# Kernel tuning notes

Hardware: AMD Instinct MI355X
Metric: run time of the kernel (lower is better)

Reference implementation:

```python
import jax, jax.numpy as jnp
import numpy as np


def setup_inputs() -> dict:
    key = jax.random.key(0)
    ks = jax.random.split(key, 8)
    B, C, H, W = 8, 256, 64, 64
    s = 1.0 / np.sqrt(C)
    return {
        "x": jax.random.normal(ks[0], (B, C, H, W), dtype=jnp.float32),
        "wq": jax.random.normal(ks[1], (C, C), dtype=jnp.float32) * s,
        "bq": jax.random.normal(ks[2], (C,), dtype=jnp.float32) * 0.01,
        "wk": jax.random.normal(ks[3], (C, C), dtype=jnp.float32) * s,
        "bk": jax.random.normal(ks[4], (C,), dtype=jnp.float32) * 0.01,
        "wv": jax.random.normal(ks[5], (C, C), dtype=jnp.float32) * s,
        "bv": jax.random.normal(ks[6], (C,), dtype=jnp.float32) * 0.01,
        "gamma": jax.random.normal(ks[7], (1,), dtype=jnp.float32) * 0.1,
    }


def reference(x, wq, bq, wk, bk, wv, bv, gamma):
    B, C, H, W = x.shape
    N = H * W
    xf = x.reshape(B, C, N)  # flatten spatial -> tokens
    # 1x1 convs == per-pixel linear maps over channels
    q = jnp.einsum('oc,bcn->bon', wq, xf) + bq[None, :, None]  # [B,C,N]
    k = jnp.einsum('oc,bcn->bon', wk, xf) + bk[None, :, None]  # [B,C,N]
    v = jnp.einsum('oc,bcn->bon', wv, xf) + bv[None, :, None]  # [B,C,N]
    # energy[b,n,m] = <q[:, n], k[:, m]>  (query tokens x key tokens)
    energy = jnp.einsum('bcn,bcm->bnm', q, k)  # [B,N,N]
    attention = jax.nn.softmax(energy, axis=-1)
    # out = V @ attention^T : out[b,c,n] = sum_m v[b,c,m] * attention[b,n,m]
    out = jnp.einsum('bcm,bnm->bcn', v, attention).reshape(B, C, H, W)
    return gamma[0] * out + x
```

## Files before the change

kernel.cpp:

```cpp
#include <hip/hip_runtime.h>
#include <hip/hip_bf16.h>
#include <cstdint>


typedef short short8 __attribute__((ext_vector_type(8)));
typedef short short4v __attribute__((ext_vector_type(4)));
typedef float f32x4 __attribute__((ext_vector_type(4)));

#define MFMA16(a, b, c) __builtin_amdgcn_mfma_f32_16x16x32_bf16((a), (b), (c), 0, 0, 0)

__device__ __forceinline__ unsigned short f2bf(float f) {
    union { float f; unsigned int u; } v;
    v.f = f;
    unsigned int u = v.u;
    return (unsigned short)((u + 0x7fffu + ((u >> 16) & 1u)) >> 16);
}

__device__ __forceinline__ void load_lds16(const unsigned short* g, unsigned short* l) {
    __builtin_amdgcn_global_load_lds(
        (const __attribute__((address_space(1))) unsigned int*)g,
        (__attribute__((address_space(3))) unsigned int*)l, 16, 0, 0);
}

__global__ __launch_bounds__(256) void wcvt_kernel(
    const float* __restrict__ wq, const float* __restrict__ wk,
    const float* __restrict__ wv, unsigned short* __restrict__ Wb)
{
    int idx = (blockIdx.x * 256 + threadIdx.x) * 4;
    const float* src = (idx < 65536) ? wq : ((idx < 131072) ? wk : wv);
    float4 f = *(const float4*)(src + (idx & 65535));
    short4v s = { (short)f2bf(f.x), (short)f2bf(f.y), (short)f2bf(f.z), (short)f2bf(f.w) };
    *(short4v*)(Wb + idx) = s;
}

__global__ __launch_bounds__(256, 2) void qkv_kernel(
    const float* __restrict__ x, const unsigned short* __restrict__ Wb,
    const float* __restrict__ bq, const float* __restrict__ bk,
    const float* __restrict__ bv,
    unsigned short* __restrict__ Qr, unsigned short* __restrict__ Kr,
    unsigned short* __restrict__ Vc)
{
    const int C = 256, N = 4096;
    __shared__ __align__(16) unsigned short Xt[32][264];

    const int tid  = threadIdx.x;
    const int bid  = blockIdx.x;
    const int b    = bid >> 7;
    const int n0   = (bid & 127) * 32;
    const int wave = tid >> 6;
    const int lane = tid & 63;
    const int quad = lane >> 4;
    const int l16  = lane & 15;
    const int ch0  = wave * 64;

    {
        const int token = tid & 31;
        const int cg    = tid >> 5;
        const float* xb = x + ((size_t)b * C) * N + n0 + token;
#pragma unroll
        for (int p = 0; p < 8; p++) {
            int c0 = p * 32 + cg * 4;
            float f0 = xb[(size_t)(c0 + 0) * N];
            float f1 = xb[(size_t)(c0 + 1) * N];
            float f2 = xb[(size_t)(c0 + 2) * N];
            float f3 = xb[(size_t)(c0 + 3) * N];
            short4v s = { (short)f2bf(f0), (short)f2bf(f1), (short)f2bf(f2), (short)f2bf(f3) };
            *(short4v*)(&Xt[token][c0]) = s;
        }
    }
    __syncthreads();

    f32x4 acc[3][4][2];
#pragma unroll
    for (int m = 0; m < 3; m++)
#pragma unroll
        for (int ct = 0; ct < 4; ct++)
#pragma unroll
            for (int tt = 0; tt < 2; tt++) acc[m][ct][tt] = (f32x4){0.f, 0.f, 0.f, 0.f};

#pragma unroll
    for (int kc = 0; kc < 8; kc++) {
        const int ko = kc * 32 + quad * 8;
        short8 ax0 = *(const short8*)(&Xt[l16][ko]);
        short8 ax1 = *(const short8*)(&Xt[16 + l16][ko]);
#pragma unroll
        for (int m = 0; m < 3; m++) {
#pragma unroll
            for (int ct = 0; ct < 4; ct++) {
                short8 wf = *(const short8*)(Wb + ((size_t)m << 16) +
                                             (ch0 + ct * 16 + l16) * 256 + ko);
                acc[m][ct][0] = MFMA16(ax0, wf, acc[m][ct][0]);
                acc[m][ct][1] = MFMA16(ax1, wf, acc[m][ct][1]);
            }
        }
    }

#pragma unroll
    for (int ct = 0; ct < 4; ct++) {
        const int ch = ch0 + ct * 16 + l16;
        const float biq = bq[ch], bik = bk[ch], biv = bv[ch];
#pragma unroll
        for (int tt = 0; tt < 2; tt++) {
            const int tok0 = n0 + tt * 16 + quad * 4;
#pragma unroll
            for (int r = 0; r < 4; r++) {
                Qr[((size_t)b * N + tok0 + r) * C + ch] = f2bf(acc[0][ct][tt][r] + biq);
                Kr[((size_t)b * N + tok0 + r) * C + ch] = f2bf(acc[1][ct][tt][r] + bik);
            }
            short4v vs = { (short)f2bf(acc[2][ct][tt][0] + biv),
                           (short)f2bf(acc[2][ct][tt][1] + biv),
                           (short)f2bf(acc[2][ct][tt][2] + biv),
                           (short)f2bf(acc[2][ct][tt][3] + biv) };
            *(short4v*)(Vc + ((size_t)b * C + ch) * N + tok0) = vs;
        }
    }
}

__global__ __launch_bounds__(512, 2) void attn_kernel(
    const unsigned short* __restrict__ Qr,
    const unsigned short* __restrict__ Kr,
    const unsigned short* __restrict__ Vc,
    const float* __restrict__ x,
    const float* __restrict__ gamma,
    float* __restrict__ out)
{
    const int C = 256, N = 4096;
    __shared__ __align__(16) unsigned short KV[2][16384];
    __shared__ __align__(16) unsigned short Pt[8][16 * 40];

    const int tid  = threadIdx.x;
    const int wave = tid >> 6;
    const int lane = tid & 63;
    const int quad = lane >> 4;
    const int l16  = lane & 15;
    const int bid  = blockIdx.x;
    const int b    = bid & 7;
    const int q0   = (bid >> 3) * 128 + wave * 16;

    const unsigned short* kb  = Kr + (size_t)b * N * C;
    const unsigned short* vcb = Vc + (size_t)b * C * N;

    short8 aq[8];
    {
        const unsigned short* qb = Qr + ((size_t)b * N + q0 + l16) * C;
#pragma unroll
        for (int f = 0; f < 8; f++)
            aq[f] = *(const short8*)(qb + f * 32 + quad * 8);
    }

    f32x4 o_acc[16];
#pragma unroll
    for (int t = 0; t < 16; t++) o_acc[t] = (f32x4){0.f, 0.f, 0.f, 0.f};
    float m_r[4], l_r[4];
#pragma unroll
    for (int r = 0; r < 4; r++) { m_r[r] = -__builtin_inff(); l_r[r] = 0.f; }

    auto stage = [&](int buf, int m0) {
        unsigned short* dst = &KV[buf][0];
#pragma unroll
        for (int p = 0; p < 2; p++) {
            int chunk = p * 512 + tid;
            int key = chunk >> 5;
            int j = (chunk & 31) ^ (key & 31);
            load_lds16(kb + (size_t)(m0 + key) * C + j * 8, dst + chunk * 8);
        }
#pragma unroll
        for (int p = 0; p < 2; p++) {
            int chunk = p * 512 + tid;
            int c = chunk >> 2;
            int j = (chunk & 3) ^ (c & 3);
            load_lds16(vcb + (size_t)c * N + m0 + j * 8, dst + 8192 + chunk * 8);
        }
    };

    stage(0, 0);
    __syncthreads();

    for (int it = 0; it < 128; ++it) {
        const int cur = it & 1;
        if (it < 127) stage(cur ^ 1, (it + 1) * 32);

        const unsigned short* Kb = &KV[cur][0];
        const unsigned short* Vb = &KV[cur][8192];

        f32x4 s0 = (f32x4){0.f, 0.f, 0.f, 0.f};
        f32x4 s1 = (f32x4){0.f, 0.f, 0.f, 0.f};
#pragma unroll
        for (int f = 0; f < 8; f++) {
            const int j = f * 4 + quad;
            int k0 = l16;
            int k1 = 16 + l16;
            short8 kf0 = *(const short8*)(Kb + (k0 * 32 + (j ^ (k0 & 31))) * 8);
            short8 kf1 = *(const short8*)(Kb + (k1 * 32 + (j ^ (k1 & 31))) * 8);
            s0 = MFMA16(aq[f], kf0, s0);
            s1 = MFMA16(aq[f], kf1, s1);
        }

        float alpha[4];
        bool anyup = false;
        unsigned short* PtW = &Pt[wave][0];
#pragma unroll
        for (int r = 0; r < 4; r++) {
            float mx = fmaxf(s0[r], s1[r]);
            mx = fmaxf(mx, __shfl_xor(mx, 1));
            mx = fmaxf(mx, __shfl_xor(mx, 2));
            mx = fmaxf(mx, __shfl_xor(mx, 4));
            mx = fmaxf(mx, __shfl_xor(mx, 8));
            float mn = fmaxf(m_r[r], mx);
            anyup |= (mn > m_r[r]);
            float al = __expf(m_r[r] - mn);
            m_r[r] = mn;
            alpha[r] = al;
            float e0 = __expf(s0[r] - mn);
            float e1 = __expf(s1[r] - mn);
            l_r[r] = l_r[r] * al + (e0 + e1);
            unsigned short* pr = PtW + (quad * 4 + r) * 40 + l16;
            pr[0]  = f2bf(e0);
            pr[16] = f2bf(e1);
        }
        if (__any(anyup)) {
            f32x4 av = (f32x4){alpha[0], alpha[1], alpha[2], alpha[3]};
#pragma unroll
            for (int t = 0; t < 16; t++) o_acc[t] *= av;
        }

        short8 ap = *(const short8*)(PtW + l16 * 40 + quad * 8);

#pragma unroll
        for (int t = 0; t < 16; t++) {
            int c = t * 16 + l16;
            short8 vf = *(const short8*)(Vb + (c * 4 + (quad ^ (c & 3))) * 8);
            o_acc[t] = MFMA16(ap, vf, o_acc[t]);
        }
        __syncthreads();
    }

    const float g = gamma[0];
    f32x4 inv;
#pragma unroll
    for (int r = 0; r < 4; r++) {
        float rs = l_r[r];
        rs += __shfl_xor(rs, 1);
        rs += __shfl_xor(rs, 2);
        rs += __shfl_xor(rs, 4);
        rs += __shfl_xor(rs, 8);
        inv[r] = g / rs;
    }
    const int nb = q0 + quad * 4;
#pragma unroll
    for (int t = 0; t < 16; t++) {
        int c = t * 16 + l16;
        size_t idx = ((size_t)(b * C + c)) * N + nb;
        f32x4 xv = *(const f32x4*)(x + idx);
        f32x4 ov = o_acc[t] * inv + xv;
        *(f32x4*)(out + idx) = ov;
    }
}

extern "C" void kernel_launch(void* const* d_in, const int* in_sizes, int n_in,
                              void* d_out, int out_size, void* d_ws, size_t ws_size,
                              hipStream_t stream) {
    const int B = 8, C = 256, N = 4096;
    const float* x     = (const float*)d_in[0];
    const float* wq    = (const float*)d_in[1];
    const float* bq    = (const float*)d_in[2];
    const float* wk    = (const float*)d_in[3];
    const float* bk    = (const float*)d_in[4];
    const float* wv    = (const float*)d_in[5];
    const float* bv    = (const float*)d_in[6];
    const float* gamma = (const float*)d_in[7];
    float* out = (float*)d_out;

    unsigned short* Qr = (unsigned short*)d_ws;
    unsigned short* Kr = Qr + (size_t)B * N * C;
    unsigned short* Vc = Kr + (size_t)B * N * C;
    unsigned short* Wb = Vc + (size_t)B * C * N;

    wcvt_kernel<<<dim3(192), 256, 0, stream>>>(wq, wk, wv, Wb);
    qkv_kernel<<<dim3(1024), 256, 0, stream>>>(x, Wb, bq, bk, bv, Qr, Kr, Vc);
    attn_kernel<<<dim3(256), 512, 0, stream>>>(Qr, Kr, Vc, x, gamma, out);
}
```

Measured before the change: 413.7 us.

## Split keys across wave groups, widen query tiles, use exp2 and wave-wide max

The attention kernel now has each wave handle 32 query rows instead of 16, so every K/V fragment loaded from LDS feeds twice as many MFMAs. The two halves of the block work on separate halves of the key sequence, split-K style, and their partial results are merged through LDS at the end. The softmax folds log2e into Q so it can use exp2f, reduces the row max once per wave with DPP, and packs bf16 conversions in pairs. The QKV kernel now writes Q channel-major and stages K through LDS for coalesced row stores. In exchange it adds register pressure (two accumulator sets), a larger LDS buffer, a combine step, and scalar strided loads for Q. A wave-wide running max may also lose precision when rows differ a lot.

```diff
diff --git a/kernel.cpp b/kernel.cpp
--- a/kernel.cpp
+++ b/kernel.cpp
@@ -8,6 +8,7 @@
 typedef float f32x4 __attribute__((ext_vector_type(4)));
 
 #define MFMA16(a, b, c) __builtin_amdgcn_mfma_f32_16x16x32_bf16((a), (b), (c), 0, 0, 0)
+#define LOG2E 1.4426950408889634f
 
 __device__ __forceinline__ unsigned short f2bf(float f) {
     union { float f; unsigned int u; } v;
@@ -20,6 +21,19 @@
     __builtin_amdgcn_global_load_lds(
         (const __attribute__((address_space(1))) unsigned int*)g,
         (__attribute__((address_space(3))) unsigned int*)l, 16, 0, 0);
+}
+
+__device__ __forceinline__ float rowmax16_dpp(float x) {
+    int v;
+    v = __builtin_amdgcn_update_dpp(0, __float_as_int(x), 0x121, 0xf, 0xf, false);
+    x = fmaxf(x, __int_as_float(v));
+    v = __builtin_amdgcn_update_dpp(0, __float_as_int(x), 0x122, 0xf, 0xf, false);
+    x = fmaxf(x, __int_as_float(v));
+    v = __builtin_amdgcn_update_dpp(0, __float_as_int(x), 0x124, 0xf, 0xf, false);
+    x = fmaxf(x, __int_as_float(v));
+    v = __builtin_amdgcn_update_dpp(0, __float_as_int(x), 0x128, 0xf, 0xf, false);
+    x = fmaxf(x, __int_as_float(v));
+    return x;
 }
 
 __global__ __launch_bounds__(256) void wcvt_kernel(
@@ -37,7 +51,7 @@
     const float* __restrict__ x, const unsigned short* __restrict__ Wb,
     const float* __restrict__ bq, const float* __restrict__ bk,
     const float* __restrict__ bv,
-    unsigned short* __restrict__ Qr, unsigned short* __restrict__ Kr,
+    unsigned short* __restrict__ Qc, unsigned short* __restrict__ Kr,
     unsigned short* __restrict__ Vc)
 {
     const int C = 256, N = 4096;
@@ -98,15 +112,15 @@
 #pragma unroll
     for (int ct = 0; ct < 4; ct++) {
         const int ch = ch0 + ct * 16 + l16;
-        const float biq = bq[ch], bik = bk[ch], biv = bv[ch];
+        const float biq = bq[ch], biv = bv[ch];
 #pragma unroll
         for (int tt = 0; tt < 2; tt++) {
             const int tok0 = n0 + tt * 16 + quad * 4;
-#pragma unroll
-            for (int r = 0; r < 4; r++) {
-                Qr[((size_t)b * N + tok0 + r) * C + ch] = f2bf(acc[0][ct][tt][r] + biq);
-                Kr[((size_t)b * N + tok0 + r) * C + ch] = f2bf(acc[1][ct][tt][r] + bik);
-            }
+            short4v qs = { (short)f2bf((acc[0][ct][tt][0] + biq) * LOG2E),
+                           (short)f2bf((acc[0][ct][tt][1] + biq) * LOG2E),
+                           (short)f2bf((acc[0][ct][tt][2] + biq) * LOG2E),
+                           (short)f2bf((acc[0][ct][tt][3] + biq) * LOG2E) };
+            *(short4v*)(Qc + ((size_t)b * C + ch) * N + tok0) = qs;
             short4v vs = { (short)f2bf(acc[2][ct][tt][0] + biv),
                            (short)f2bf(acc[2][ct][tt][1] + biv),
                            (short)f2bf(acc[2][ct][tt][2] + biv),
@@ -114,10 +128,31 @@
             *(short4v*)(Vc + ((size_t)b * C + ch) * N + tok0) = vs;
         }
     }
+
+    __syncthreads();
+#pragma unroll
+    for (int ct = 0; ct < 4; ct++) {
+        const int ch = ch0 + ct * 16 + l16;
+        const float bik = bk[ch];
+#pragma unroll
+        for (int tt = 0; tt < 2; tt++) {
+#pragma unroll
+            for (int r = 0; r < 4; r++)
+                Xt[tt * 16 + quad * 4 + r][ch] = f2bf(acc[1][ct][tt][r] + bik);
+        }
+    }
+    __syncthreads();
+#pragma unroll
+    for (int p = 0; p < 2; p++) {
+        int chunk = p * 256 + tid;
+        int tok = chunk >> 4;
+        int cc  = (chunk & 15) * 16;
+        *(short8*)(Kr + ((size_t)b * N + n0 + tok) * C + cc) = *(const short8*)(&Xt[tok][cc]);
+    }
 }
 
 __global__ __launch_bounds__(512, 2) void attn_kernel(
-    const unsigned short* __restrict__ Qr,
+    const unsigned short* __restrict__ Qc,
     const unsigned short* __restrict__ Kr,
     const unsigned short* __restrict__ Vc,
     const float* __restrict__ x,
@@ -125,135 +160,220 @@
     float* __restrict__ out)
 {
     const int C = 256, N = 4096;
-    __shared__ __align__(16) unsigned short KV[2][16384];
-    __shared__ __align__(16) unsigned short Pt[8][16 * 40];
+    __shared__ __align__(16) unsigned short KV[2][32768];
+    __shared__ __align__(16) unsigned short Pt[8][1280];
+    __shared__ float MlL[4][32];
+    __shared__ float MwL[4];
 
     const int tid  = threadIdx.x;
     const int wave = tid >> 6;
+    const int ks   = wave >> 2;
+    const int w4   = wave & 3;
     const int lane = tid & 63;
     const int quad = lane >> 4;
     const int l16  = lane & 15;
     const int bid  = blockIdx.x;
     const int b    = bid & 7;
-    const int q0   = (bid >> 3) * 128 + wave * 16;
+    const int q0   = (bid >> 3) * 128 + w4 * 32;
 
     const unsigned short* kb  = Kr + (size_t)b * N * C;
     const unsigned short* vcb = Vc + (size_t)b * C * N;
 
-    short8 aq[8];
+    short8 aqL[8], aqH[8];
     {
-        const unsigned short* qb = Qr + ((size_t)b * N + q0 + l16) * C;
-#pragma unroll
-        for (int f = 0; f < 8; f++)
-            aq[f] = *(const short8*)(qb + f * 32 + quad * 8);
-    }
-
-    f32x4 o_acc[16];
-#pragma unroll
-    for (int t = 0; t < 16; t++) o_acc[t] = (f32x4){0.f, 0.f, 0.f, 0.f};
-    float m_r[4], l_r[4];
-#pragma unroll
-    for (int r = 0; r < 4; r++) { m_r[r] = -__builtin_inff(); l_r[r] = 0.f; }
+        const unsigned short* qb = Qc + (size_t)b * C * N + q0 + l16;
+#pragma unroll
+        for (int f = 0; f < 8; f++) {
+#pragma unroll
+            for (int j = 0; j < 8; j++) {
+                size_t co = (size_t)(f * 32 + quad * 8 + j) * N;
+                aqL[f][j] = (short)qb[co];
+                aqH[f][j] = (short)qb[co + 16];
+            }
+        }
+    }
+
+    f32x4 oL[16], oH[16];
+#pragma unroll
+    for (int t = 0; t < 16; t++) {
+        oL[t] = (f32x4){0.f, 0.f, 0.f, 0.f};
+        oH[t] = (f32x4){0.f, 0.f, 0.f, 0.f};
+    }
+    float m_w = -__builtin_inff();
+    float l_p[2][4];
+#pragma unroll
+    for (int h = 0; h < 2; h++)
+#pragma unroll
+        for (int r = 0; r < 4; r++) l_p[h][r] = 0.f;
 
     auto stage = [&](int buf, int m0) {
         unsigned short* dst = &KV[buf][0];
 #pragma unroll
-        for (int p = 0; p < 2; p++) {
+        for (int p = 0; p < 4; p++) {
             int chunk = p * 512 + tid;
-            int key = chunk >> 5;
-            int j = (chunk & 31) ^ (key & 31);
-            load_lds16(kb + (size_t)(m0 + key) * C + j * 8, dst + chunk * 8);
-        }
-#pragma unroll
-        for (int p = 0; p < 2; p++) {
+            int half = chunk >> 10;
+            int idx  = chunk & 1023;
+            int key = idx >> 5;
+            int j = (idx & 31) ^ (key & 31);
+            load_lds16(kb + (size_t)(half * 2048 + m0 + key) * C + j * 8,
+                       dst + half * 16384 + idx * 8);
+        }
+#pragma unroll
+        for (int p = 0; p < 4; p++) {
             int chunk = p * 512 + tid;
-            int c = chunk >> 2;
-            int j = (chunk & 3) ^ (c & 3);
-            load_lds16(vcb + (size_t)c * N + m0 + j * 8, dst + 8192 + chunk * 8);
+            int half = chunk >> 10;
+            int idx  = chunk & 1023;
+            int c = idx >> 2;
+            int j = (idx & 3) ^ (c & 3);
+            load_lds16(vcb + (size_t)c * N + half * 2048 + m0 + j * 8,
+                       dst + half * 16384 + 8192 + idx * 8);
         }
     };
 
     stage(0, 0);
     __syncthreads();
 
-    for (int it = 0; it < 128; ++it) {
+    unsigned short* PtW = &Pt[wave][0];
+
+    for (int it = 0; it < 64; ++it) {
         const int cur = it & 1;
-        if (it < 127) stage(cur ^ 1, (it + 1) * 32);
-
-        const unsigned short* Kb = &KV[cur][0];
-        const unsigned short* Vb = &KV[cur][8192];
-
-        f32x4 s0 = (f32x4){0.f, 0.f, 0.f, 0.f};
-        f32x4 s1 = (f32x4){0.f, 0.f, 0.f, 0.f};
+        if (it < 63) stage(cur ^ 1, (it + 1) * 32);
+
+        const unsigned short* Kb = &KV[cur][ks * 16384];
+        const unsigned short* Vb = Kb + 8192;
+
+        f32x4 sL0 = {0.f,0.f,0.f,0.f}, sL1 = {0.f,0.f,0.f,0.f};
+        f32x4 sH0 = {0.f,0.f,0.f,0.f}, sH1 = {0.f,0.f,0.f,0.f};
 #pragma unroll
         for (int f = 0; f < 8; f++) {
             const int j = f * 4 + quad;
-            int k0 = l16;
-            int k1 = 16 + l16;
+            int k0 = l16, k1 = 16 + l16;
             short8 kf0 = *(const short8*)(Kb + (k0 * 32 + (j ^ (k0 & 31))) * 8);
             short8 kf1 = *(const short8*)(Kb + (k1 * 32 + (j ^ (k1 & 31))) * 8);
-            s0 = MFMA16(aq[f], kf0, s0);
-            s1 = MFMA16(aq[f], kf1, s1);
-        }
-
-        float alpha[4];
-        bool anyup = false;
-        unsigned short* PtW = &Pt[wave][0];
+            sL0 = MFMA16(aqL[f], kf0, sL0);
+            sL1 = MFMA16(aqL[f], kf1, sL1);
+            sH0 = MFMA16(aqH[f], kf0, sH0);
+            sH1 = MFMA16(aqH[f], kf1, sH1);
+        }
+
+        float mx = fmaxf(fmaxf(fmaxf(sL0[0], sL0[1]), fmaxf(sL0[2], sL0[3])),
+                         fmaxf(fmaxf(sL1[0], sL1[1]), fmaxf(sL1[2], sL1[3])));
+        mx = fmaxf(mx, fmaxf(fmaxf(fmaxf(sH0[0], sH0[1]), fmaxf(sH0[2], sH0[3])),
+                             fmaxf(fmaxf(sH1[0], sH1[1]), fmaxf(sH1[2], sH1[3]))));
+        mx = rowmax16_dpp(mx);
+        mx = fmaxf(mx, __shfl_xor(mx, 16));
+        mx = fmaxf(mx, __shfl_xor(mx, 32));
+        const float mn = fmaxf(m_w, mx);
+        const float al = exp2f(m_w - mn);
+        const bool up = mn > m_w;
+        m_w = mn;
+
 #pragma unroll
         for (int r = 0; r < 4; r++) {
-            float mx = fmaxf(s0[r], s1[r]);
-            mx = fmaxf(mx, __shfl_xor(mx, 1));
-            mx = fmaxf(mx, __shfl_xor(mx, 2));
-            mx = fmaxf(mx, __shfl_xor(mx, 4));
-            mx = fmaxf(mx, __shfl_xor(mx, 8));
-            float mn = fmaxf(m_r[r], mx);
-            anyup |= (mn > m_r[r]);
-            float al = __expf(m_r[r] - mn);
-            m_r[r] = mn;
-            alpha[r] = al;
-            float e0 = __expf(s0[r] - mn);
-            float e1 = __expf(s1[r] - mn);
-            l_r[r] = l_r[r] * al + (e0 + e1);
-            unsigned short* pr = PtW + (quad * 4 + r) * 40 + l16;
-            pr[0]  = f2bf(e0);
-            pr[16] = f2bf(e1);
-        }
-        if (__any(anyup)) {
-            f32x4 av = (f32x4){alpha[0], alpha[1], alpha[2], alpha[3]};
-#pragma unroll
-            for (int t = 0; t < 16; t++) o_acc[t] *= av;
-        }
-
-        short8 ap = *(const short8*)(PtW + l16 * 40 + quad * 8);
+            {
+                float e0 = exp2f(sL0[r] - mn);
+                float e1 = exp2f(sL1[r] - mn);
+                l_p[0][r] = l_p[0][r] * al + (e0 + e1);
+                union { __hip_bfloat162 v; unsigned int u; } cv;
+                cv.v = __float22bfloat162_rn(float2{e0, e1});
+                unsigned short* pr = PtW + (quad * 4 + r) * 40 + l16;
+                pr[0]  = (unsigned short)(cv.u & 0xffff);
+                pr[16] = (unsigned short)(cv.u >> 16);
+            }
+            {
+                float e0 = exp2f(sH0[r] - mn);
+                float e1 = exp2f(sH1[r] - mn);
+                l_p[1][r] = l_p[1][r] * al + (e0 + e1);
+                union { __hip_bfloat162 v; unsigned int u; } cv;
+                cv.v = __float22bfloat162_rn(float2{e0, e1});
+                unsigned short* pr = PtW + (16 + quad * 4 + r) * 40 + l16;
+                pr[0]  = (unsigned short)(cv.u & 0xffff);
+                pr[16] = (unsigned short)(cv.u >> 16);
+            }
+        }
+        if (up) {
+#pragma unroll
+            for (int t = 0; t < 16; t++) { oL[t] *= al; oH[t] *= al; }
+        }
+
+        short8 apL = *(const short8*)(PtW + l16 * 40 + quad * 8);
+        short8 apH = *(const short8*)(PtW + (16 + l16) * 40 + quad * 8);
 
 #pragma unroll
         for (int t = 0; t < 16; t++) {
             int c = t * 16 + l16;
             short8 vf = *(const short8*)(Vb + (c * 4 + (quad ^ (c & 3))) * 8);
-            o_acc[t] = MFMA16(ap, vf, o_acc[t]);
+            oL[t] = MFMA16(apL, vf, oL[t]);
+            oH[t] = MFMA16(apH, vf, oH[t]);
         }
         __syncthreads();
     }
 
-    const float g = gamma[0];
-    f32x4 inv;
-#pragma unroll
-    for (int r = 0; r < 4; r++) {
-        float rs = l_r[r];
-        rs += __shfl_xor(rs, 1);
-        rs += __shfl_xor(rs, 2);
-        rs += __shfl_xor(rs, 4);
-        rs += __shfl_xor(rs, 8);
-        inv[r] = g / rs;
-    }
-    const int nb = q0 + quad * 4;
-#pragma unroll
-    for (int t = 0; t < 16; t++) {
-        int c = t * 16 + l16;
-        size_t idx = ((size_t)(b * C + c)) * N + nb;
-        f32x4 xv = *(const f32x4*)(x + idx);
-        f32x4 ov = o_acc[t] * inv + xv;
-        *(f32x4*)(out + idx) = ov;
+#pragma unroll
+    for (int h = 0; h < 2; h++)
+#pragma unroll
+        for (int r = 0; r < 4; r++) {
+            float rs = l_p[h][r];
+            rs += __shfl_xor(rs, 1);
+            rs += __shfl_xor(rs, 2);
+            rs += __shfl_xor(rs, 4);
+            rs += __shfl_xor(rs, 8);
+            l_p[h][r] = rs;
+        }
+
+    float* CombF = (float*)(&KV[0][0]);
+    __syncthreads();
+    if (ks == 1) {
+#pragma unroll
+        for (int t = 0; t < 16; t++) {
+#pragma unroll
+            for (int r = 0; r < 4; r++) {
+                CombF[(size_t)(w4 * 32 + quad * 4 + r) * 256 + t * 16 + l16] = oL[t][r];
+                CombF[(size_t)(w4 * 32 + 16 + quad * 4 + r) * 256 + t * 16 + l16] = oH[t][r];
+            }
+        }
+        if (l16 == 0) {
+#pragma unroll
+            for (int h = 0; h < 2; h++)
+#pragma unroll
+                for (int r = 0; r < 4; r++)
+                    MlL[w4][h * 16 + quad * 4 + r] = l_p[h][r];
+            if (lane == 0) MwL[w4] = m_w;
+        }
+    }
+    __syncthreads();
+    if (ks == 0) {
+        const float g = gamma[0];
+        const float m2w = MwL[w4];
+        const float mt = fmaxf(m_w, m2w);
+        const float f1 = exp2f(m_w - mt);
+        const float f2 = exp2f(m2w - mt);
+        float linv[2][4];
+#pragma unroll
+        for (int h = 0; h < 2; h++)
+#pragma unroll
+            for (int r = 0; r < 4; r++) {
+                float l2 = MlL[w4][h * 16 + quad * 4 + r];
+                linv[h][r] = g / (l_p[h][r] * f1 + l2 * f2);
+            }
+#pragma unroll
+        for (int t = 0; t < 16; t++) {
+            const int c = t * 16 + l16;
+#pragma unroll
+            for (int h = 0; h < 2; h++) {
+                const int nb = q0 + h * 16 + quad * 4;
+                f32x4 o1 = h ? oH[t] : oL[t];
+                f32x4 ov;
+#pragma unroll
+                for (int r = 0; r < 4; r++) {
+                    float o2 = CombF[(size_t)(w4 * 32 + h * 16 + quad * 4 + r) * 256 + c];
+                    ov[r] = (o1[r] * f1 + o2 * f2) * linv[h][r];
+                }
+                size_t idx = ((size_t)(b * C + c)) * N + nb;
+                f32x4 xv = *(const f32x4*)(x + idx);
+                *(f32x4*)(out + idx) = ov + xv;
+            }
+        }
     }
 }
 
@@ -271,12 +391,12 @@
     const float* gamma = (const float*)d_in[7];
     float* out = (float*)d_out;
 
-    unsigned short* Qr = (unsigned short*)d_ws;
-    unsigned short* Kr = Qr + (size_t)B * N * C;
+    unsigned short* Qc = (unsigned short*)d_ws;
+    unsigned short* Kr = Qc + (size_t)B * C * N;
     unsigned short* Vc = Kr + (size_t)B * N * C;
     unsigned short* Wb = Vc + (size_t)B * C * N;
 
     wcvt_kernel<<<dim3(192), 256, 0, stream>>>(wq, wk, wv, Wb);
-    qkv_kernel<<<dim3(1024), 256, 0, stream>>>(x, Wb, bq, bk, bv, Qr, Kr, Vc);
-    attn_kernel<<<dim3(256), 512, 0, stream>>>(Qr, Kr, Vc, x, gamma, out);
-}
+    qkv_kernel<<<dim3(1024), 256, 0, stream>>>(x, Wb, bq, bk, bv, Qc, Kr, Vc);
+    attn_kernel<<<dim3(256), 512, 0, stream>>>(Qc, Kr, Vc, x, gamma, out);
+}
```

Result: faster. 393.6 us (-4.9%).
